# Performance work log

Hardware: AMD Instinct MI355X
Metric: run time of the kernel (lower is better)

The kernel has to match this reference:

```python
import jax, jax.numpy as jnp
import numpy as np
import math

EMBED_DIM = 1024
N_HEAD = 16
HEAD_DIM = EMBED_DIM // N_HEAD


def setup_inputs() -> dict:
    key = jax.random.key(0)
    ks = jax.random.split(key, 9)
    B, T, C = 4, 2048, EMBED_DIM
    s = 1.0 / math.sqrt(C)
    return {
        "x": jax.random.normal(ks[0], (B, T, C), dtype=jnp.float32),
        "Wq": jax.random.normal(ks[1], (C, C), dtype=jnp.float32) * s,
        "bq": jnp.zeros((C,), dtype=jnp.float32),
        "Wk": jax.random.normal(ks[2], (C, C), dtype=jnp.float32) * s,
        "bk": jnp.zeros((C,), dtype=jnp.float32),
        "Wv": jax.random.normal(ks[3], (C, C), dtype=jnp.float32) * s,
        "bv": jnp.zeros((C,), dtype=jnp.float32),
        "Wp": jax.random.normal(ks[4], (C, C), dtype=jnp.float32) * s,
        "bp": jnp.zeros((C,), dtype=jnp.float32),
    }


def reference(x, Wq, bq, Wk, bk, Wv, bv, Wp, bp):
    B, T, C = x.shape
    H, D = N_HEAD, HEAD_DIM

    def heads(W, b):
        # [B,T,C] -> [B,H,T,D]
        return (x @ W.T + b).reshape(B, T, H, D).transpose(0, 2, 1, 3)

    q = heads(Wq, bq)
    k = heads(Wk, bk)
    v = heads(Wv, bv)

    att = jnp.einsum("bhtd,bhsd->bhts", q, k) * (1.0 / math.sqrt(D))
    causal = jnp.tril(jnp.ones((T, T), dtype=bool))
    att = jnp.where(causal[None, None], att, -jnp.inf)
    att = jax.nn.softmax(att, axis=-1)
    y = jnp.einsum("bhts,bhsd->bhtd", att, v)  # [B,H,T,D]
    y = y.transpose(0, 2, 1, 3).reshape(B, T, C)
    return y @ Wp.T + bp
```

## Files before the change

kernel.cpp:

```cpp
#include <hip/hip_runtime.h>
#include <hip/hip_bf16.h>
#include <cstdint>
#include <cstddef>

#define TQ 2048
#define CDIM 1024
#define NH 16
#define HD 64

typedef __attribute__((ext_vector_type(8))) short bf16x8;
typedef __attribute__((ext_vector_type(4))) float f32x4;
typedef __attribute__((ext_vector_type(16))) float f32x16;

__device__ __forceinline__ unsigned short f2bf(float f) {
  union { float f; unsigned u; } x; x.f = f;
  unsigned r = x.u + 0x7fffu + ((x.u >> 16) & 1u);
  return (unsigned short)(r >> 16);
}

__device__ __forceinline__ unsigned cvtpk(float lo, float hi) {
  unsigned r;
  asm("v_cvt_pk_bf16_f32 %0, %1, %2" : "=v"(r) : "v"(lo), "v"(hi));
  return r;
}

__device__ __forceinline__ void plswap(unsigned& x, unsigned& y) {
  asm("v_permlane32_swap_b32 %0, %1" : "+v"(x), "+v"(y));
}

__device__ __forceinline__ float exp2_fast(float x) {
  float r;
  asm("v_exp_f32 %0, %1" : "=v"(r) : "v"(x));
  return r;
}

__device__ __forceinline__ void gload_lds16(const void* g, void* l) {
  typedef __attribute__((address_space(1))) const void gv;
  typedef __attribute__((address_space(3))) void lv;
  __builtin_amdgcn_global_load_lds((gv*)g, (lv*)l, 16, 0, 0);
}

#define BAR() do { asm volatile("" ::: "memory"); __builtin_amdgcn_s_barrier(); asm volatile("" ::: "memory"); } while (0)
#define VMC2() asm volatile("s_waitcnt vmcnt(2)" ::: "memory")
#define VMC0() asm volatile("s_waitcnt vmcnt(0)" ::: "memory")

__global__ void cvt_bf16_kernel(const float* __restrict__ in,
                                unsigned short* __restrict__ out, int n) {
  int stride = gridDim.x * blockDim.x;
  for (int i = blockIdx.x * blockDim.x + threadIdx.x; i * 4 < n; i += stride) {
    float4 v = *(const float4*)(in + (size_t)i * 4);
    ushort4 o;
    o.x = f2bf(v.x); o.y = f2bf(v.y); o.z = f2bf(v.z); o.w = f2bf(v.w);
    *(ushort4*)(out + (size_t)i * 4) = o;
  }
}

__global__ void cvt4_kernel(const float* __restrict__ w0, const float* __restrict__ w1,
                            const float* __restrict__ w2, const float* __restrict__ w3,
                            unsigned short* __restrict__ out) {
  int i = blockIdx.x * blockDim.x + threadIdx.x;
  int which = i >> 18;
  const float* src = which == 0 ? w0 : which == 1 ? w1 : which == 2 ? w2 : w3;
  int off = (i & 262143) * 4;
  float4 v = *(const float4*)(src + off);
  ushort4 o;
  o.x = f2bf(v.x); o.y = f2bf(v.y); o.z = f2bf(v.z); o.w = f2bf(v.w);
  *(ushort4*)(out + (size_t)i * 4) = o;
}

template <int EPI>
__global__ __launch_bounds__(512, 2) void gemm256_kernel(
    const unsigned short* __restrict__ A,
    const unsigned short* __restrict__ Bt,
    const float* __restrict__ b0, const float* __restrict__ b1,
    void* __restrict__ outp,
    int M, int N, int K) {
  __shared__ __align__(16) char lds[131072];

  const int tid = (int)threadIdx.x;
  const int w = tid >> 6, lane = tid & 63;
  const int g = lane >> 4, c = lane & 15;
  const int wm = w >> 2, wn = w & 3;

  const int nbm = M >> 8, nbn = N >> 8;
  const int nwg = nbm * nbn;
  int id = (int)blockIdx.x;
  const int cpx = nwg >> 3;
  id = (id & 7) * cpx + (id >> 3);
  const int tm = id % nbm, tn = id / nbm;

  const char* Ab = (const char*)(A + (size_t)tm * 256 * K);
  const char* Bb = (const char*)(Bt + (size_t)tn * 256 * K);
  const int rowB = K * 2;
  const int nht = (K >> 6) << 2;

  char* aw = lds + wm * 16384;
  char* bw = lds + 65536 + (wn >> 1) * 16384;
  const int bfo = (wn & 1) * 8;

  auto stage_ht = [&](int j) {
    if (j >= nht) return;
    const int t = j >> 2, part = j & 3;
    const int isB = part >> 1, half = part & 1;
    const char* src = isB ? Bb : Ab;
    char* dst = lds + isB * 65536 + (t & 1) * 32768 + half * 16384 + w * 2048;
#pragma unroll
    for (int r = 0; r < 2; ++r) {
      const int f = w * 2 + r;
      const int m16 = f >> 1, ki = f & 1;
      gload_lds16(src + (size_t)(half * 128 + m16 * 16 + c) * rowB +
                      t * 128 + ki * 64 + g * 16,
                  dst + r * 1024);
    }
  };

  f32x4 acc[8][4];
#pragma unroll
  for (int i = 0; i < 8; ++i)
#pragma unroll
    for (int j = 0; j < 4; ++j) acc[i][j] = (f32x4){0.f, 0.f, 0.f, 0.f};
  bf16x8 af[4][2], bv[2][2];

  auto rdA = [&](int buf, int ms) {
#pragma unroll
    for (int mi = 0; mi < 4; ++mi)
#pragma unroll
      for (int ki = 0; ki < 2; ++ki)
        af[mi][ki] = *(const bf16x8*)(aw + buf * 32768 +
                                      ((ms * 4 + mi) * 2 + ki) * 1024 + lane * 16);
  };
  auto rdB = [&](int buf, int ns) {
#pragma unroll
    for (int ni = 0; ni < 2; ++ni)
#pragma unroll
      for (int ki = 0; ki < 2; ++ki)
        bv[ni][ki] = *(const bf16x8*)(bw + buf * 32768 +
                                      (bfo + (ns * 2 + ni) * 2 + ki) * 1024 + lane * 16);
  };
  auto mm = [&](int ms, int ns) {
    __builtin_amdgcn_s_setprio(1);
#pragma unroll
    for (int mi = 0; mi < 4; ++mi)
#pragma unroll
      for (int ni = 0; ni < 2; ++ni)
#pragma unroll
        for (int ki = 0; ki < 2; ++ki)
          acc[ms * 4 + mi][ns * 2 + ni] = __builtin_amdgcn_mfma_f32_16x16x32_bf16(
              af[mi][ki], bv[ni][ki], acc[ms * 4 + mi][ns * 2 + ni], 0, 0, 0);
    __builtin_amdgcn_s_setprio(0);
  };

  for (int j = 0; j < 5; ++j) stage_ht(j);
  VMC2();
  BAR();

  const int niter = K >> 7;
#pragma unroll 1
  for (int i = 0; i < niter; ++i) {
    const int j0 = 5 + (i << 3);
    rdA(0, 0); rdB(0, 0); stage_ht(j0 + 0); BAR(); mm(0, 0); BAR();
    rdB(0, 1);            stage_ht(j0 + 1); BAR(); mm(0, 1); BAR();
    rdA(0, 1);            stage_ht(j0 + 2); BAR(); mm(1, 1); BAR();
    rdB(0, 0);            stage_ht(j0 + 3);
    if (i + 1 < niter) { VMC2(); } else { VMC0(); }
    BAR(); mm(1, 0); BAR();
    rdA(1, 0); rdB(1, 0); stage_ht(j0 + 4); BAR(); mm(0, 0); BAR();
    rdB(1, 1);            stage_ht(j0 + 5); BAR(); mm(0, 1); BAR();
    rdA(1, 1);            stage_ht(j0 + 6); BAR(); mm(1, 1); BAR();
    rdB(1, 0);            stage_ht(j0 + 7); VMC2(); BAR(); mm(1, 0); BAR();
  }

#pragma unroll
  for (int mi = 0; mi < 8; ++mi) {
#pragma unroll
    for (int ni = 0; ni < 4; ++ni) {
      const int n = tn * 256 + wn * 64 + ni * 16 + c;
#pragma unroll
      for (int e = 0; e < 4; ++e) {
        const int m = tm * 256 + wm * 128 + mi * 16 + g * 4 + e;
        float v = acc[mi][ni][e];
        if (EPI == 1) {
          v += b0[m];
          size_t idx = ((size_t)(n >> 11) * (NH * HD) + m) * TQ + (n & (TQ - 1));
          ((unsigned short*)outp)[idx] = f2bf(v);
        } else if (EPI == 2) {
          v += b0[n];
          ((float*)outp)[(size_t)m * N + n] = v;
        } else {
          unsigned short* O = (unsigned short*)outp;
          if (n < 1024) {
            v = (v + b0[n]) * 0.18033688f;
            size_t idx = ((size_t)(m >> 11) * NH + (n >> 6)) * (TQ * HD) +
                         (size_t)(m & (TQ - 1)) * HD + (n & (HD - 1));
            O[idx] = f2bf(v);
          } else {
            int nn = n - 1024;
            v += b1[nn];
            size_t idx = 8388608 + ((size_t)(m >> 11) * NH + (nn >> 6)) * (TQ * HD) +
                         (size_t)(m & (TQ - 1)) * HD + (nn & (HD - 1));
            O[idx] = f2bf(v);
          }
        }
      }
    }
  }
}

__global__ __launch_bounds__(256, 4) void attn_kernel(
    const unsigned short* __restrict__ Q,
    const unsigned short* __restrict__ K,
    const unsigned short* __restrict__ Vt,
    unsigned short* __restrict__ Y) {
  __shared__ __align__(16) char Ks[2][8192];
  __shared__ __align__(16) char Vs[2][8192];

  const int tid = (int)threadIdx.x;
  const int w = tid >> 6, lane = tid & 63;
  const int l31 = lane & 31, hi = lane >> 5;

  const int n = (int)blockIdx.x;
  const int g = n & 255, k = n >> 8;
  const int bh = g >> 2;
  const int u = 2 * (g & 3) + (k >> 1);
  const int qt = (k & 1) ? (15 - u) : u;
  const int b = bh >> 4, h = bh & 15;

  const unsigned short* Qb = Q + (size_t)bh * TQ * HD;
  const char* Kb = (const char*)(K + (size_t)bh * TQ * HD);
  const char* Vb = (const char*)(Vt + (size_t)bh * HD * TQ);

  auto stage = [&](int buf, int kt) {
#pragma unroll
    for (int i = 0; i < 2; ++i) {
      const int s = i * 256 + tid;
      const int r32 = (s >> 8) * 32 + (s & 31);
      const int ck = ((s >> 6) & 3) * 32 + ((s >> 5) & 1) * 16;
      char* kdst = &Ks[buf][0] + i * 4096 + (w << 10);
      char* vdst = &Vs[buf][0] + i * 4096 + (w << 10);
      gload_lds16(Kb + (size_t)kt * 8192 + r32 * 128 + ck, kdst);
      gload_lds16(Vb + (size_t)r32 * 4096 + kt * 128 + ck, vdst);
    }
  };

  const int q0 = qt * 128 + w * 32;
  const int qg = q0 + l31;
  const int nkv = 2 * qt + 2;

  stage(0, 0);

  bf16x8 qf[4];
#pragma unroll
  for (int dk = 0; dk < 4; ++dk)
    qf[dk] = *(const bf16x8*)(Qb + (size_t)qg * HD + dk * 16 + hi * 8);

  f32x16 oac[2];
#pragma unroll
  for (int nb = 0; nb < 2; ++nb)
#pragma unroll
    for (int r = 0; r < 16; ++r) oac[nb][r] = 0.f;
  float mr = -3.0e38f, lr = 0.f;

  __syncthreads();

  for (int kt = 0; kt < nkv; ++kt) {
    const int cur = kt & 1;
    if (kt + 1 < nkv) stage(cur ^ 1, kt + 1);

    if (kt * 64 <= q0 + 31) {
      const char* Klane = &Ks[cur][0] + lane * 16;
      const char* Vlane = &Vs[cur][0] + lane * 16;

      f32x16 s0, s1;
#pragma unroll
      for (int r = 0; r < 16; ++r) { s0[r] = 0.f; s1[r] = 0.f; }
#pragma unroll
      for (int dk = 0; dk < 4; ++dk) {
        bf16x8 kf0 = *(const bf16x8*)(Klane + (dk << 10));
        bf16x8 kf1 = *(const bf16x8*)(Klane + ((4 + dk) << 10));
        s0 = __builtin_amdgcn_mfma_f32_32x32x16_bf16(kf0, qf[dk], s0, 0, 0, 0);
        s1 = __builtin_amdgcn_mfma_f32_32x32x16_bf16(kf1, qf[dk], s1, 0, 0, 0);
      }

      const bool maskT = (kt * 64 + 63 > q0);
      if (maskT) {
#pragma unroll
        for (int r = 0; r < 16; ++r) {
          int kv0 = kt * 64 + ((r & 3) + 8 * (r >> 2)) + 4 * hi;
          s0[r] = (kv0 <= qg) ? s0[r] : -3.0e38f;
          s1[r] = (kv0 + 32 <= qg) ? s1[r] : -3.0e38f;
        }
      }

      float mt_ = s0[0];
#pragma unroll
      for (int r = 1; r < 16; ++r) mt_ = fmaxf(mt_, s0[r]);
#pragma unroll
      for (int r = 0; r < 16; ++r) mt_ = fmaxf(mt_, s1[r]);
      mt_ = fmaxf(mt_, __shfl_xor(mt_, 32));

      if (!__all(mt_ - mr <= 8.0f)) {
        const float mn = fmaxf(mr, mt_);
        const float al = exp2_fast(mr - mn);
        mr = mn;
        lr *= al;
#pragma unroll
        for (int nb = 0; nb < 2; ++nb)
#pragma unroll
          for (int r = 0; r < 16; ++r) oac[nb][r] *= al;
      }

      float rs = 0.f;
#pragma unroll
      for (int r = 0; r < 16; ++r) { s0[r] = exp2_fast(s0[r] - mr); rs += s0[r]; }
#pragma unroll
      for (int r = 0; r < 16; ++r) { s1[r] = exp2_fast(s1[r] - mr); rs += s1[r]; }
      rs += __shfl_xor(rs, 32);
      lr += rs;

      bf16x8 pf[4];
      {
        unsigned a0 = cvtpk(s0[0], s0[1]), b0 = cvtpk(s0[2], s0[3]);
        unsigned c0 = cvtpk(s0[4], s0[5]), d0 = cvtpk(s0[6], s0[7]);
        plswap(a0, c0); plswap(b0, d0);
        unsigned a1 = cvtpk(s0[8], s0[9]), b1 = cvtpk(s0[10], s0[11]);
        unsigned c1 = cvtpk(s0[12], s0[13]), d1 = cvtpk(s0[14], s0[15]);
        plswap(a1, c1); plswap(b1, d1);
        unsigned a2 = cvtpk(s1[0], s1[1]), b2 = cvtpk(s1[2], s1[3]);
        unsigned c2 = cvtpk(s1[4], s1[5]), d2 = cvtpk(s1[6], s1[7]);
        plswap(a2, c2); plswap(b2, d2);
        unsigned a3 = cvtpk(s1[8], s1[9]), b3 = cvtpk(s1[10], s1[11]);
        unsigned c3 = cvtpk(s1[12], s1[13]), d3 = cvtpk(s1[14], s1[15]);
        plswap(a3, c3); plswap(b3, d3);
        union { unsigned u[4]; bf16x8 v; } t;
        t.u[0] = a0; t.u[1] = b0; t.u[2] = c0; t.u[3] = d0; pf[0] = t.v;
        t.u[0] = a1; t.u[1] = b1; t.u[2] = c1; t.u[3] = d1; pf[1] = t.v;
        t.u[0] = a2; t.u[1] = b2; t.u[2] = c2; t.u[3] = d2; pf[2] = t.v;
        t.u[0] = a3; t.u[1] = b3; t.u[2] = c3; t.u[3] = d3; pf[3] = t.v;
      }

#pragma unroll
      for (int nb = 0; nb < 2; ++nb)
#pragma unroll
        for (int ks = 0; ks < 4; ++ks) {
          bf16x8 vf = *(const bf16x8*)(Vlane + (((nb << 2) + ks) << 10));
          oac[nb] = __builtin_amdgcn_mfma_f32_32x32x16_bf16(vf, pf[ks], oac[nb], 0, 0, 0);
        }
    }
    __syncthreads();
  }

  float inv;
  asm("v_rcp_f32 %0, %1" : "=v"(inv) : "v"(lr));
  unsigned short* Yrow = Y + (size_t)(b * TQ + qg) * CDIM + h * 64;
#pragma unroll
  for (int nb = 0; nb < 2; ++nb)
#pragma unroll
    for (int j = 0; j < 8; ++j) {
      const int dbase = ((2 * j) & 3) + 8 * (j >> 1);
      unsigned lo = f2bf(oac[nb][2 * j] * inv);
      unsigned hi2 = f2bf(oac[nb][2 * j + 1] * inv);
      *(unsigned*)(Yrow + nb * 32 + dbase + 4 * hi) = lo | (hi2 << 16);
    }
}

extern "C" void kernel_launch(void* const* d_in, const int* in_sizes, int n_in,
                              void* d_out, int out_size, void* d_ws, size_t ws_size,
                              hipStream_t stream) {
  (void)in_sizes; (void)n_in; (void)out_size; (void)ws_size;
  const float* x  = (const float*)d_in[0];
  const float* Wq = (const float*)d_in[1];
  const float* bq = (const float*)d_in[2];
  const float* Wk = (const float*)d_in[3];
  const float* bk = (const float*)d_in[4];
  const float* Wv = (const float*)d_in[5];
  const float* bv = (const float*)d_in[6];
  const float* Wp = (const float*)d_in[7];
  const float* bp = (const float*)d_in[8];
  float* out = (float*)d_out;

  char* ws = (char*)d_ws;
  unsigned short* xb  = (unsigned short*)(ws + 0);
  unsigned short* wqb = (unsigned short*)(ws + 16777216);
  unsigned short* wvb = (unsigned short*)(ws + 20971520);
  unsigned short* wpb = (unsigned short*)(ws + 23068672);
  unsigned short* Qh  = (unsigned short*)(ws + 25165824);
  unsigned short* Kh  = (unsigned short*)(ws + 41943040);
  unsigned short* Vt  = (unsigned short*)(ws + 58720256);
  unsigned short* y   = (unsigned short*)(ws + 75497472);

  const int nx = 4 * TQ * CDIM;

  cvt_bf16_kernel<<<4096, 256, 0, stream>>>(x, xb, nx);
  cvt4_kernel<<<4096, 256, 0, stream>>>(Wq, Wk, Wv, Wp, wqb);

  gemm256_kernel<4><<<256, 512, 0, stream>>>(xb, wqb, bq, bk, Qh, 8192, 2048, 1024);
  gemm256_kernel<1><<<128, 512, 0, stream>>>(wvb, xb, bv, bv, Vt, 1024, 8192, 1024);

  attn_kernel<<<1024, 256, 0, stream>>>(Qh, Kh, Vt, y);

  gemm256_kernel<2><<<128, 512, 0, stream>>>(y, wpb, bp, bp, out, 8192, 1024, 1024);
}
```

Measured before the change: 218.3 us.

## Shrink GEMM tile to 128x256 and restructure LDS staging pipeline

Replaces the 256x256 GEMM tile with a 128x256 tile, cutting LDS use to 96 KB and doubling the number of workgroups so the 256-CU device is better filled (128-block launches become 256, 256 become 512). The staging and compute schedule is rewritten around separate A and B loads with double buffering per K-tile. In exchange, per-block arithmetic intensity drops and global traffic for the B operand roughly doubles.

```diff
diff --git a/kernel.cpp b/kernel.cpp
--- a/kernel.cpp
+++ b/kernel.cpp
@@ -69,115 +69,116 @@
 }
 
 template <int EPI>
-__global__ __launch_bounds__(512, 2) void gemm256_kernel(
+__global__ __launch_bounds__(512, 2) void gemm128x256_kernel(
     const unsigned short* __restrict__ A,
     const unsigned short* __restrict__ Bt,
     const float* __restrict__ b0, const float* __restrict__ b1,
     void* __restrict__ outp,
     int M, int N, int K) {
-  __shared__ __align__(16) char lds[131072];
+  __shared__ __align__(16) char lds[98304];
 
   const int tid = (int)threadIdx.x;
   const int w = tid >> 6, lane = tid & 63;
   const int g = lane >> 4, c = lane & 15;
   const int wm = w >> 2, wn = w & 3;
 
-  const int nbm = M >> 8, nbn = N >> 8;
+  const int nbm = M >> 7, nbn = N >> 8;
   const int nwg = nbm * nbn;
   int id = (int)blockIdx.x;
   const int cpx = nwg >> 3;
   id = (id & 7) * cpx + (id >> 3);
   const int tm = id % nbm, tn = id / nbm;
 
-  const char* Ab = (const char*)(A + (size_t)tm * 256 * K);
+  const char* Ab = (const char*)(A + (size_t)tm * 128 * K);
   const char* Bb = (const char*)(Bt + (size_t)tn * 256 * K);
   const int rowB = K * 2;
-  const int nht = (K >> 6) << 2;
-
-  char* aw = lds + wm * 16384;
-  char* bw = lds + 65536 + (wn >> 1) * 16384;
-  const int bfo = (wn & 1) * 8;
-
-  auto stage_ht = [&](int j) {
-    if (j >= nht) return;
-    const int t = j >> 2, part = j & 3;
-    const int isB = part >> 1, half = part & 1;
-    const char* src = isB ? Bb : Ab;
-    char* dst = lds + isB * 65536 + (t & 1) * 32768 + half * 16384 + w * 2048;
-#pragma unroll
-    for (int r = 0; r < 2; ++r) {
-      const int f = w * 2 + r;
-      const int m16 = f >> 1, ki = f & 1;
-      gload_lds16(src + (size_t)(half * 128 + m16 * 16 + c) * rowB +
-                      t * 128 + ki * 64 + g * 16,
-                  dst + r * 1024);
-    }
-  };
-
-  f32x4 acc[8][4];
-#pragma unroll
-  for (int i = 0; i < 8; ++i)
+  const int nt = K >> 6;
+
+  auto stageA = [&](int t) {
+    if (t >= nt) return;
+    char* dst = lds + (t & 1) * 49152 + (w << 11);
+    const char* s = Ab + (size_t)(w * 16 + c) * rowB + t * 128 + g * 16;
+    gload_lds16(s, dst);
+    gload_lds16(s + 64, dst + 1024);
+  };
+  auto stageB = [&](int t, int odd) {
+    if (t >= nt) return;
+    const int n16 = (w >> 1) * 4 + 2 * odd + (w & 1);
+    char* dst = lds + (t & 1) * 49152 + 16384 + (n16 << 11);
+    const char* s = Bb + (size_t)(n16 * 16 + c) * rowB + t * 128 + g * 16;
+    gload_lds16(s, dst);
+    gload_lds16(s + 64, dst + 1024);
+  };
+
+  f32x4 acc[4][4];
+#pragma unroll
+  for (int i = 0; i < 4; ++i)
 #pragma unroll
     for (int j = 0; j < 4; ++j) acc[i][j] = (f32x4){0.f, 0.f, 0.f, 0.f};
-  bf16x8 af[4][2], bv[2][2];
-
-  auto rdA = [&](int buf, int ms) {
-#pragma unroll
-    for (int mi = 0; mi < 4; ++mi)
+  bf16x8 af[2][2], bv[2][2][2];
+
+  auto rdA = [&](int cur, int ms) {
+#pragma unroll
+    for (int mi2 = 0; mi2 < 2; ++mi2)
 #pragma unroll
       for (int ki = 0; ki < 2; ++ki)
-        af[mi][ki] = *(const bf16x8*)(aw + buf * 32768 +
-                                      ((ms * 4 + mi) * 2 + ki) * 1024 + lane * 16);
-  };
-  auto rdB = [&](int buf, int ns) {
-#pragma unroll
-    for (int ni = 0; ni < 2; ++ni)
+        af[mi2][ki] = *(const bf16x8*)(lds + cur * 49152 +
+            (((wm * 4 + ms * 2 + mi2) << 1) + ki) * 1024 + lane * 16);
+  };
+  auto rdB = [&](int cur, int ns) {
+#pragma unroll
+    for (int ni2 = 0; ni2 < 2; ++ni2)
 #pragma unroll
       for (int ki = 0; ki < 2; ++ki)
-        bv[ni][ki] = *(const bf16x8*)(bw + buf * 32768 +
-                                      (bfo + (ns * 2 + ni) * 2 + ki) * 1024 + lane * 16);
+        bv[ns][ni2][ki] = *(const bf16x8*)(lds + cur * 49152 + 16384 +
+            (((wn * 4 + ns * 2 + ni2) << 1) + ki) * 1024 + lane * 16);
   };
   auto mm = [&](int ms, int ns) {
     __builtin_amdgcn_s_setprio(1);
 #pragma unroll
-    for (int mi = 0; mi < 4; ++mi)
-#pragma unroll
-      for (int ni = 0; ni < 2; ++ni)
+    for (int mi2 = 0; mi2 < 2; ++mi2)
+#pragma unroll
+      for (int ni2 = 0; ni2 < 2; ++ni2)
 #pragma unroll
         for (int ki = 0; ki < 2; ++ki)
-          acc[ms * 4 + mi][ns * 2 + ni] = __builtin_amdgcn_mfma_f32_16x16x32_bf16(
-              af[mi][ki], bv[ni][ki], acc[ms * 4 + mi][ns * 2 + ni], 0, 0, 0);
+          acc[ms * 2 + mi2][ns * 2 + ni2] = __builtin_amdgcn_mfma_f32_16x16x32_bf16(
+              af[mi2][ki], bv[ns][ni2][ki], acc[ms * 2 + mi2][ns * 2 + ni2], 0, 0, 0);
     __builtin_amdgcn_s_setprio(0);
   };
 
-  for (int j = 0; j < 5; ++j) stage_ht(j);
+  stageA(0); stageB(0, 0); stageB(0, 1);
   VMC2();
   BAR();
 
-  const int niter = K >> 7;
 #pragma unroll 1
-  for (int i = 0; i < niter; ++i) {
-    const int j0 = 5 + (i << 3);
-    rdA(0, 0); rdB(0, 0); stage_ht(j0 + 0); BAR(); mm(0, 0); BAR();
-    rdB(0, 1);            stage_ht(j0 + 1); BAR(); mm(0, 1); BAR();
-    rdA(0, 1);            stage_ht(j0 + 2); BAR(); mm(1, 1); BAR();
-    rdB(0, 0);            stage_ht(j0 + 3);
-    if (i + 1 < niter) { VMC2(); } else { VMC0(); }
-    BAR(); mm(1, 0); BAR();
-    rdA(1, 0); rdB(1, 0); stage_ht(j0 + 4); BAR(); mm(0, 0); BAR();
-    rdB(1, 1);            stage_ht(j0 + 5); BAR(); mm(0, 1); BAR();
-    rdA(1, 1);            stage_ht(j0 + 6); BAR(); mm(1, 1); BAR();
-    rdB(1, 0);            stage_ht(j0 + 7); VMC2(); BAR(); mm(1, 0); BAR();
+  for (int i = 0; i < (nt >> 1); ++i) {
+    const int t0 = 2 * i, t1 = 2 * i + 1;
+    rdA(0, 0); rdB(0, 0); stageA(t0 + 1);
+    mm(0, 0); VMC2(); BAR();
+    rdB(0, 1); stageB(t0 + 1, 0);
+    mm(0, 1); BAR();
+    rdA(0, 1); stageB(t0 + 1, 1);
+    mm(1, 1); BAR();
+    mm(1, 0); VMC2(); BAR();
+    rdA(1, 0); rdB(1, 0); stageA(t1 + 1);
+    mm(0, 0);
+    if (t1 == nt - 1) { VMC0(); } else { VMC2(); }
+    BAR();
+    rdB(1, 1); stageB(t1 + 1, 0);
+    mm(0, 1); BAR();
+    rdA(1, 1); stageB(t1 + 1, 1);
+    mm(1, 1); BAR();
+    mm(1, 0); VMC2(); BAR();
   }
 
 #pragma unroll
-  for (int mi = 0; mi < 8; ++mi) {
+  for (int mi = 0; mi < 4; ++mi) {
 #pragma unroll
     for (int ni = 0; ni < 4; ++ni) {
       const int n = tn * 256 + wn * 64 + ni * 16 + c;
 #pragma unroll
       for (int e = 0; e < 4; ++e) {
-        const int m = tm * 256 + wm * 128 + mi * 16 + g * 4 + e;
+        const int m = tm * 128 + wm * 64 + mi * 16 + g * 4 + e;
         float v = acc[mi][ni][e];
         if (EPI == 1) {
           v += b0[m];
@@ -393,10 +394,10 @@
   cvt_bf16_kernel<<<4096, 256, 0, stream>>>(x, xb, nx);
   cvt4_kernel<<<4096, 256, 0, stream>>>(Wq, Wk, Wv, Wp, wqb);
 
-  gemm256_kernel<4><<<256, 512, 0, stream>>>(xb, wqb, bq, bk, Qh, 8192, 2048, 1024);
-  gemm256_kernel<1><<<128, 512, 0, stream>>>(wvb, xb, bv, bv, Vt, 1024, 8192, 1024);
+  gemm128x256_kernel<4><<<512, 512, 0, stream>>>(xb, wqb, bq, bk, Qh, 8192, 2048, 1024);
+  gemm128x256_kernel<1><<<256, 512, 0, stream>>>(wvb, xb, bv, bv, Vt, 1024, 8192, 1024);
 
   attn_kernel<<<1024, 256, 0, stream>>>(Qh, Kh, Vt, y);
 
-  gemm256_kernel<2><<<128, 512, 0, stream>>>(y, wpb, bp, bp, out, 8192, 1024, 1024);
-}
+  gemm128x256_kernel<2><<<256, 512, 0, stream>>>(y, wpb, bp, bp, out, 8192, 1024, 1024);
+}
```

After: 209.4 us. -4.1%, faster.
